# Optimization experiments

Hardware: AMD Instinct MI355X
Metric: run time of the kernel (lower is better)

The kernel has to match this reference:

```python
import jax, jax.numpy as jnp
import numpy as np

B, C_IN, C_OUT, N, K = 16, 128, 128, 4096, 16


def setup_inputs() -> dict:
    key = jax.random.key(0)
    k1, k2, k3, k4 = jax.random.split(key, 4)
    x = jax.random.normal(k1, (B, C_IN, N, 1), dtype=jnp.float32)
    edge_index = jax.random.randint(k2, (2, B, N, K), 0, N, dtype=jnp.int32)
    # 1x1 conv weight of BasicConv([C_IN, C_OUT], 'relu', None, bias=False)
    W = jax.random.normal(k3, (C_OUT, C_IN), dtype=jnp.float32) * (1.0 / np.sqrt(C_IN))
    # module bias param, initialized to zeros; use random here to exercise the add
    bias = jax.random.normal(k4, (1, C_OUT, 1, 1), dtype=jnp.float32) * 0.01
    return {"x": x, "edge_index": edge_index, "W": W, "bias": bias}


def reference(x, edge_index, W, bias):
    b, _, n, _ = x.shape
    # BasicConv: 1x1 conv (no bias) + ReLU
    h = jax.nn.relu(jnp.einsum('oi,binu->bonu', W, x))  # [B, C_out, N, 1]
    h2 = h[..., 0]                                       # [B, C_out, N]
    # add_self_loops: append self index along neighbor dim
    self_idx = jnp.broadcast_to(jnp.arange(n, dtype=edge_index.dtype)[None, None, :, None],
                                (2, b, n, 1))
    ei = jnp.concatenate([edge_index, self_idx], axis=-1)  # [2, B, N, K+1]
    idx = ei[0]                                            # [B, N, K+1]
    deg = ei.shape[-1]
    norm = 1.0 / deg
    # batched_index_select: gather neighbor features -> [B, C_out, N, K+1]
    x_j = jax.vmap(lambda hb, ib: hb[:, ib])(h2, idx)
    aggr = (x_j * norm).sum(axis=-1, keepdims=True)        # [B, C_out, N, 1]
    return aggr + bias
```

## Files before the change

kernel.cpp:

```cpp
#include <hip/hip_runtime.h>

#define B_    16
#define CIN_  128
#define COUT_ 128
#define N_    4096
#define K_    16

typedef __attribute__((ext_vector_type(8))) short bf16x8;
typedef __attribute__((ext_vector_type(4))) float f32x4;

__device__ inline unsigned short f2bf(float f) {
  unsigned u = __float_as_uint(f);
  u += 0x7fffu + ((u >> 16) & 1u);
  return (unsigned short)(u >> 16);
}

__device__ inline void swizzle(int l, int& b, int& n0) {
  int xcd = l & 7, slot = l >> 3;
  b  = (xcd << 1) | (slot >> 6);
  n0 = (slot & 63) * 64;
}

__global__ __launch_bounds__(256) void gemm_relu_k(
    const float* __restrict__ x, const float* __restrict__ W,
    unsigned short* __restrict__ h) {
  __shared__ unsigned short Wl[128 * 136];
  const int tid = threadIdx.x;
  int b, n0;
  swizzle(blockIdx.x, b, n0);

#pragma unroll
  for (int r = 0; r < 16; ++r) {
    int id = tid + 256 * r;
    int co = id >> 5;
    int cq = id & 31;
    float4 v = reinterpret_cast<const float4*>(W)[id];
    unsigned p0 = (unsigned)f2bf(v.x) | ((unsigned)f2bf(v.y) << 16);
    unsigned p1 = (unsigned)f2bf(v.z) | ((unsigned)f2bf(v.w) << 16);
    *reinterpret_cast<uint2*>(&Wl[co * 136 + 4 * cq]) = make_uint2(p0, p1);
  }
  __syncthreads();

  const int lane = tid & 63;
  const int w    = tid >> 6;
  const int m    = lane & 15;
  const int quad = lane >> 4;

  const float* xb = x + (size_t)b * CIN_ * N_ + n0 + 16 * w + m;
  bf16x8 a[4];
#pragma unroll
  for (int s = 0; s < 4; ++s) {
#pragma unroll
    for (int j = 0; j < 8; ++j) {
      int ci = 32 * s + 8 * quad + j;
      a[s][j] = (short)f2bf(xb[(size_t)ci * N_]);
    }
  }

  const int nrow_base = n0 + 16 * w + 4 * quad;
  unsigned short* hb = h + (size_t)b * N_ * COUT_;
#pragma unroll
  for (int t = 0; t < 8; ++t) {
    f32x4 c = {0.f, 0.f, 0.f, 0.f};
#pragma unroll
    for (int s = 0; s < 4; ++s) {
      bf16x8 bf = *reinterpret_cast<const bf16x8*>(
          &Wl[(16 * t + m) * 136 + 32 * s + 8 * quad]);
      c = __builtin_amdgcn_mfma_f32_16x16x32_bf16(a[s], bf, c, 0, 0, 0);
    }
    int co = 16 * t + m;
#pragma unroll
    for (int r = 0; r < 4; ++r) {
      float v = c[r] > 0.f ? c[r] : 0.f;
      hb[(size_t)(nrow_base + r) * COUT_ + co] = f2bf(v);
    }
  }
}

__global__ __launch_bounds__(256) void aggr_k(
    const unsigned short* __restrict__ h, const int* __restrict__ ei,
    const float* __restrict__ bias, float* __restrict__ out) {
  __shared__ int idx_s[64 * K_];
  const int tid = threadIdx.x;
  int b, n0;
  swizzle(blockIdx.x, b, n0);

  {
    const int4* src =
        reinterpret_cast<const int4*>(ei + ((size_t)b * N_ + n0) * K_);
    reinterpret_cast<int4*>(idx_s)[tid] = src[tid];
  }
  __syncthreads();

  const int q = tid & 31;
  const int g = tid >> 5;
  const unsigned short* hb = h + (size_t)b * N_ * COUT_;

  float acc[8][4];
#pragma unroll
  for (int j = 0; j < 8; ++j) {
    uint2 v = *reinterpret_cast<const uint2*>(
        hb + (size_t)(n0 + 8 * g + j) * COUT_ + 4 * q);
    acc[j][0] = __uint_as_float(v.x << 16);
    acc[j][1] = __uint_as_float(v.x & 0xffff0000u);
    acc[j][2] = __uint_as_float(v.y << 16);
    acc[j][3] = __uint_as_float(v.y & 0xffff0000u);
  }
  for (int k = 0; k < K_; ++k) {
#pragma unroll
    for (int j = 0; j < 8; ++j) {
      int jj = idx_s[(8 * g + j) * K_ + k];
      uint2 v = *reinterpret_cast<const uint2*>(
          hb + (size_t)jj * COUT_ + 4 * q);
      acc[j][0] += __uint_as_float(v.x << 16);
      acc[j][1] += __uint_as_float(v.x & 0xffff0000u);
      acc[j][2] += __uint_as_float(v.y << 16);
      acc[j][3] += __uint_as_float(v.y & 0xffff0000u);
    }
  }

  const float norm = 1.0f / 17.0f;
  const float4 bv = *reinterpret_cast<const float4*>(bias + 4 * q);
  float* ob = out + (size_t)b * COUT_ * N_ + n0 + 8 * g;
#pragma unroll
  for (int r = 0; r < 4; ++r) {
    int co = 4 * q + r;
    float bb = (r == 0) ? bv.x : (r == 1) ? bv.y : (r == 2) ? bv.z : bv.w;
    float4 lo, hi;
    lo.x = acc[0][r] * norm + bb; lo.y = acc[1][r] * norm + bb;
    lo.z = acc[2][r] * norm + bb; lo.w = acc[3][r] * norm + bb;
    hi.x = acc[4][r] * norm + bb; hi.y = acc[5][r] * norm + bb;
    hi.z = acc[6][r] * norm + bb; hi.w = acc[7][r] * norm + bb;
    *reinterpret_cast<float4*>(ob + (size_t)co * N_)     = lo;
    *reinterpret_cast<float4*>(ob + (size_t)co * N_ + 4) = hi;
  }
}

extern "C" void kernel_launch(void* const* d_in, const int* in_sizes, int n_in,
                              void* d_out, int out_size, void* d_ws, size_t ws_size,
                              hipStream_t stream) {
  const float* x    = (const float*)d_in[0];
  const int*   ei   = (const int*)d_in[1];
  const float* W    = (const float*)d_in[2];
  const float* bias = (const float*)d_in[3];
  float* out = (float*)d_out;
  unsigned short* h = (unsigned short*)d_ws;

  gemm_relu_k<<<dim3(B_ * N_ / 64), 256, 0, stream>>>(x, W, h);
  aggr_k<<<dim3(B_ * N_ / 64), 256, 0, stream>>>(h, ei, bias, out);
}
```

Baseline: 124.2 us.

## Retile GEMM to 128 rows per block and split gather into two phased launches

The GEMM now processes 128 nodes per block with two MFMA accumulators per wave, so each staged copy of W in LDS is reused over more rows. The aggregation kernel changes from 64 to 32 nodes per block, uses 16-byte gathers over 8 channels, and stores neighbor indices transposed in LDS. It also switches to nontemporal index loads and output stores, and runs as two launches of 8 batches each so each phase's gather working set stays in cache. The XCD-aware swizzle is dropped in favour of plain mapping, and the extra launch adds fixed overhead.

```diff
diff --git a/kernel.cpp b/kernel.cpp
--- a/kernel.cpp
+++ b/kernel.cpp
@@ -8,6 +8,8 @@
 
 typedef __attribute__((ext_vector_type(8))) short bf16x8;
 typedef __attribute__((ext_vector_type(4))) float f32x4;
+typedef __attribute__((ext_vector_type(4))) int   i32x4;
+typedef __attribute__((ext_vector_type(2))) float f32x2;
 
 __device__ inline unsigned short f2bf(float f) {
   unsigned u = __float_as_uint(f);
@@ -15,19 +17,13 @@
   return (unsigned short)(u >> 16);
 }
 
-__device__ inline void swizzle(int l, int& b, int& n0) {
-  int xcd = l & 7, slot = l >> 3;
-  b  = (xcd << 1) | (slot >> 6);
-  n0 = (slot & 63) * 64;
-}
-
 __global__ __launch_bounds__(256) void gemm_relu_k(
     const float* __restrict__ x, const float* __restrict__ W,
     unsigned short* __restrict__ h) {
   __shared__ unsigned short Wl[128 * 136];
   const int tid = threadIdx.x;
-  int b, n0;
-  swizzle(blockIdx.x, b, n0);
+  const int b   = blockIdx.x >> 5;
+  const int n0  = (blockIdx.x & 31) * 128;
 
 #pragma unroll
   for (int r = 0; r < 16; ++r) {
@@ -46,93 +42,113 @@
   const int m    = lane & 15;
   const int quad = lane >> 4;
 
-  const float* xb = x + (size_t)b * CIN_ * N_ + n0 + 16 * w + m;
-  bf16x8 a[4];
+  const float* xb = x + (size_t)b * CIN_ * N_ + n0 + 32 * w + m;
+  bf16x8 a[2][4];
 #pragma unroll
-  for (int s = 0; s < 4; ++s) {
+  for (int p = 0; p < 2; ++p) {
 #pragma unroll
-    for (int j = 0; j < 8; ++j) {
-      int ci = 32 * s + 8 * quad + j;
-      a[s][j] = (short)f2bf(xb[(size_t)ci * N_]);
+    for (int s = 0; s < 4; ++s) {
+#pragma unroll
+      for (int j = 0; j < 8; ++j) {
+        int ci = 32 * s + 8 * quad + j;
+        a[p][s][j] = (short)f2bf(xb[(size_t)ci * N_ + 16 * p]);
+      }
     }
   }
 
-  const int nrow_base = n0 + 16 * w + 4 * quad;
   unsigned short* hb = h + (size_t)b * N_ * COUT_;
+  const int rbase = n0 + 32 * w + 4 * quad;
 #pragma unroll
   for (int t = 0; t < 8; ++t) {
-    f32x4 c = {0.f, 0.f, 0.f, 0.f};
+    f32x4 c0 = {0.f, 0.f, 0.f, 0.f}, c1 = c0;
 #pragma unroll
     for (int s = 0; s < 4; ++s) {
       bf16x8 bf = *reinterpret_cast<const bf16x8*>(
           &Wl[(16 * t + m) * 136 + 32 * s + 8 * quad]);
-      c = __builtin_amdgcn_mfma_f32_16x16x32_bf16(a[s], bf, c, 0, 0, 0);
+      c0 = __builtin_amdgcn_mfma_f32_16x16x32_bf16(a[0][s], bf, c0, 0, 0, 0);
+      c1 = __builtin_amdgcn_mfma_f32_16x16x32_bf16(a[1][s], bf, c1, 0, 0, 0);
     }
     int co = 16 * t + m;
 #pragma unroll
     for (int r = 0; r < 4; ++r) {
-      float v = c[r] > 0.f ? c[r] : 0.f;
-      hb[(size_t)(nrow_base + r) * COUT_ + co] = f2bf(v);
+      float v0 = c0[r] > 0.f ? c0[r] : 0.f;
+      float v1 = c1[r] > 0.f ? c1[r] : 0.f;
+      hb[(size_t)(rbase + r) * COUT_ + co]      = f2bf(v0);
+      hb[(size_t)(rbase + 16 + r) * COUT_ + co] = f2bf(v1);
     }
   }
 }
 
 __global__ __launch_bounds__(256) void aggr_k(
     const unsigned short* __restrict__ h, const int* __restrict__ ei,
-    const float* __restrict__ bias, float* __restrict__ out) {
-  __shared__ int idx_s[64 * K_];
+    const float* __restrict__ bias, float* __restrict__ out, int phase) {
+  __shared__ int idx_t[K_ * 32];
   const int tid = threadIdx.x;
-  int b, n0;
-  swizzle(blockIdx.x, b, n0);
+  const int b   = 8 * phase + (blockIdx.x & 7);
+  const int n0  = (blockIdx.x >> 3) * 32;
 
-  {
-    const int4* src =
-        reinterpret_cast<const int4*>(ei + ((size_t)b * N_ + n0) * K_);
-    reinterpret_cast<int4*>(idx_s)[tid] = src[tid];
+  if (tid < 128) {
+    int n  = tid >> 2;
+    int kq = tid & 3;
+    i32x4 v = __builtin_nontemporal_load(
+        reinterpret_cast<const i32x4*>(ei + ((size_t)b * N_ + n0 + n) * K_) + kq);
+    idx_t[(4 * kq + 0) * 32 + n] = v.x;
+    idx_t[(4 * kq + 1) * 32 + n] = v.y;
+    idx_t[(4 * kq + 2) * 32 + n] = v.z;
+    idx_t[(4 * kq + 3) * 32 + n] = v.w;
   }
   __syncthreads();
 
-  const int q = tid & 31;
-  const int g = tid >> 5;
+  const int q = tid & 15;
+  const int g = tid >> 4;
   const unsigned short* hb = h + (size_t)b * N_ * COUT_;
 
-  float acc[8][4];
+  float acc[2][8];
 #pragma unroll
-  for (int j = 0; j < 8; ++j) {
-    uint2 v = *reinterpret_cast<const uint2*>(
-        hb + (size_t)(n0 + 8 * g + j) * COUT_ + 4 * q);
+  for (int j = 0; j < 2; ++j) {
+    uint4 v = *reinterpret_cast<const uint4*>(
+        hb + (size_t)(n0 + 2 * g + j) * COUT_ + 8 * q);
     acc[j][0] = __uint_as_float(v.x << 16);
     acc[j][1] = __uint_as_float(v.x & 0xffff0000u);
     acc[j][2] = __uint_as_float(v.y << 16);
     acc[j][3] = __uint_as_float(v.y & 0xffff0000u);
+    acc[j][4] = __uint_as_float(v.z << 16);
+    acc[j][5] = __uint_as_float(v.z & 0xffff0000u);
+    acc[j][6] = __uint_as_float(v.w << 16);
+    acc[j][7] = __uint_as_float(v.w & 0xffff0000u);
   }
+#pragma unroll 4
   for (int k = 0; k < K_; ++k) {
+    int2 jj = *reinterpret_cast<const int2*>(&idx_t[k * 32 + 2 * g]);
 #pragma unroll
-    for (int j = 0; j < 8; ++j) {
-      int jj = idx_s[(8 * g + j) * K_ + k];
-      uint2 v = *reinterpret_cast<const uint2*>(
-          hb + (size_t)jj * COUT_ + 4 * q);
+    for (int j = 0; j < 2; ++j) {
+      int node = (j == 0) ? jj.x : jj.y;
+      uint4 v = *reinterpret_cast<const uint4*>(
+          hb + (size_t)node * COUT_ + 8 * q);
       acc[j][0] += __uint_as_float(v.x << 16);
       acc[j][1] += __uint_as_float(v.x & 0xffff0000u);
       acc[j][2] += __uint_as_float(v.y << 16);
       acc[j][3] += __uint_as_float(v.y & 0xffff0000u);
+      acc[j][4] += __uint_as_float(v.z << 16);
+      acc[j][5] += __uint_as_float(v.z & 0xffff0000u);
+      acc[j][6] += __uint_as_float(v.w << 16);
+      acc[j][7] += __uint_as_float(v.w & 0xffff0000u);
     }
   }
 
   const float norm = 1.0f / 17.0f;
-  const float4 bv = *reinterpret_cast<const float4*>(bias + 4 * q);
-  float* ob = out + (size_t)b * COUT_ * N_ + n0 + 8 * g;
+  const float4 bv0 = *reinterpret_cast<const float4*>(bias + 8 * q);
+  const float4 bv1 = *reinterpret_cast<const float4*>(bias + 8 * q + 4);
+  float* ob = out + (size_t)b * COUT_ * N_ + n0 + 2 * g;
 #pragma unroll
-  for (int r = 0; r < 4; ++r) {
-    int co = 4 * q + r;
-    float bb = (r == 0) ? bv.x : (r == 1) ? bv.y : (r == 2) ? bv.z : bv.w;
-    float4 lo, hi;
-    lo.x = acc[0][r] * norm + bb; lo.y = acc[1][r] * norm + bb;
-    lo.z = acc[2][r] * norm + bb; lo.w = acc[3][r] * norm + bb;
-    hi.x = acc[4][r] * norm + bb; hi.y = acc[5][r] * norm + bb;
-    hi.z = acc[6][r] * norm + bb; hi.w = acc[7][r] * norm + bb;
-    *reinterpret_cast<float4*>(ob + (size_t)co * N_)     = lo;
-    *reinterpret_cast<float4*>(ob + (size_t)co * N_ + 4) = hi;
+  for (int c = 0; c < 8; ++c) {
+    int co = 8 * q + c;
+    float bb = (c < 4) ? ((c == 0) ? bv0.x : (c == 1) ? bv0.y : (c == 2) ? bv0.z : bv0.w)
+                       : ((c == 4) ? bv1.x : (c == 5) ? bv1.y : (c == 6) ? bv1.z : bv1.w);
+    f32x2 r;
+    r.x = acc[0][c] * norm + bb;
+    r.y = acc[1][c] * norm + bb;
+    __builtin_nontemporal_store(r, reinterpret_cast<f32x2*>(ob + (size_t)co * N_));
   }
 }
 
@@ -146,6 +162,7 @@
   float* out = (float*)d_out;
   unsigned short* h = (unsigned short*)d_ws;
 
-  gemm_relu_k<<<dim3(B_ * N_ / 64), 256, 0, stream>>>(x, W, h);
-  aggr_k<<<dim3(B_ * N_ / 64), 256, 0, stream>>>(h, ei, bias, out);
+  gemm_relu_k<<<dim3(B_ * N_ / 128), 256, 0, stream>>>(x, W, h);
+  aggr_k<<<dim3(8 * (N_ / 32)), 256, 0, stream>>>(h, ei, bias, out, 0);
+  aggr_k<<<dim3(8 * (N_ / 32)), 256, 0, stream>>>(h, ei, bias, out, 1);
 }
```

After: 130.2 us. +4.9%, slower.
